# Optimization experiments

Hardware: AMD Instinct MI355X
Metric: run time of the kernel (lower is better)

## Reference

```python
import jax, jax.numpy as jnp
import numpy as np

N_NODES = 50000
N_EDGES = 800000
F_IN = 128
HID = 128
N_CLASSES = 16
N_GRAPHS = 64


def _glorot(key, shape):
    fan_in, fan_out = shape[0], shape[1]
    lim = (6.0 / (fan_in + fan_out)) ** 0.5
    return jax.random.uniform(key, shape, jnp.float32, -lim, lim)


def setup_inputs() -> dict:
    key = jax.random.key(0)
    ks = jax.random.split(key, 12)
    x = jax.random.normal(ks[0], (N_NODES, F_IN), jnp.float32)
    edge_index = jax.random.randint(ks[1], (2, N_EDGES), 0, N_NODES, jnp.int64)
    batch = jnp.sort(jax.random.randint(ks[2], (N_NODES,), 0, N_GRAPHS, jnp.int64))
    W0 = _glorot(ks[3], (F_IN, HID)); b0 = jnp.zeros((HID,), jnp.float32)
    W1 = _glorot(ks[4], (HID, HID)); b1 = jnp.zeros((HID,), jnp.float32)
    W2 = _glorot(ks[5], (HID, HID)); b2 = jnp.zeros((HID,), jnp.float32)
    Wc = _glorot(ks[6], (HID, N_CLASSES)); bc = jnp.zeros((N_CLASSES,), jnp.float32)
    return {"x": x, "edge_index": edge_index, "batch": batch,
            "W0": W0, "b0": b0, "W1": W1, "b1": b1, "W2": W2, "b2": b2,
            "Wc": Wc, "bc": bc}


def _gcn_prep(edge_index, n_nodes):
    # add self-loops, compute symmetric normalization coefficients
    loop = jnp.arange(n_nodes, dtype=edge_index.dtype)
    src = jnp.concatenate([edge_index[0], loop])
    dst = jnp.concatenate([edge_index[1], loop])
    deg = jax.ops.segment_sum(jnp.ones_like(dst, jnp.float32), dst, num_segments=n_nodes)
    dinv = deg ** -0.5  # deg >= 1 due to self-loops
    norm = dinv[src] * dinv[dst]  # [E+N]
    return src, dst, norm


def _gcn_layer(h, W, b, src, dst, norm, n_nodes):
    h = h @ W                                   # [N, out]
    msg = h[src] * norm[:, None]                # gather + scale [E+N, out]
    out = jax.ops.segment_sum(msg, dst, num_segments=n_nodes)  # scatter-add
    return out + b


def reference(x, edge_index, batch, W0, b0, W1, b1, W2, b2, Wc, bc):
    n = x.shape[0]
    src, dst, norm = _gcn_prep(edge_index, n)
    h = _gcn_layer(x, W0, b0, src, dst, norm, n)
    h = jax.nn.relu(h)  # dropout is identity in eval mode
    h = _gcn_layer(h, W1, b1, src, dst, norm, n)
    h = jax.nn.relu(h)
    h = _gcn_layer(h, W2, b2, src, dst, norm, n)
    # scatter-mean pooling over batch ids
    sums = jax.ops.segment_sum(h, batch, num_segments=N_GRAPHS)        # [G, HID]
    cnts = jax.ops.segment_sum(jnp.ones((n,), jnp.float32), batch, num_segments=N_GRAPHS)
    pooled = sums / jnp.maximum(cnts, 1.0)[:, None]
    return pooled @ Wc + bc  # [G, N_CLASSES]
```

## Files before the change

### kernel.cpp

```cpp
#include <hip/hip_runtime.h>
#include <hip/hip_bf16.h>
#include <hip/hip_fp16.h>

#define HID 128
#define NCLS 16
#define NGRAPH 64
#define CHUNK 1024

using bf16x8 = __attribute__((ext_vector_type(8))) short;
using f32x4  = __attribute__((ext_vector_type(4))) float;

__device__ __forceinline__ unsigned int f2bf(float f) {
    unsigned int u = __float_as_uint(f);
    return (u + 0x7FFFu + ((u >> 16) & 1u)) >> 16;
}
__device__ __forceinline__ float bf2f_lo(unsigned int u) { return __uint_as_float(u << 16); }
__device__ __forceinline__ float bf2f_hi(unsigned int u) { return __uint_as_float(u & 0xFFFF0000u); }

__global__ __launch_bounds__(256) void k_init(int* counts, float* pooled,
                                              const float* __restrict__ W0,
                                              const float* __restrict__ W1,
                                              const float* __restrict__ W2,
                                              const float* __restrict__ Wc,
                                              const float* __restrict__ b2,
                                              const float* __restrict__ bcin,
                                              unsigned short* __restrict__ Wt,
                                              unsigned short* __restrict__ Wt2c,
                                              float* __restrict__ bc2, int n) {
    int i = blockIdx.x * 256 + threadIdx.x;
    if (i < n) counts[i] = 0;
    if (i < NGRAPH * NCLS) pooled[i] = 0.0f;
    if (i < 2 * HID * HID) {
        int m = i >> 14;
        int r = i & 16383;
        int c = r >> 7, k = r & 127;
        const float* W = (m == 0) ? W0 : W1;
        Wt[i] = (unsigned short)f2bf(W[k * HID + c]);
    }
    if (i < HID * NCLS) {
        int k = i >> 4, c = i & 15;
        float s = 0.f;
        #pragma unroll 8
        for (int j = 0; j < HID; ++j)
            s = fmaf(W2[k * HID + j], Wc[j * NCLS + c], s);
        Wt2c[c * 128 + k] = (unsigned short)f2bf(s);
    }
    if (i < NCLS) {
        float s = 0.f;
        for (int j = 0; j < HID; ++j)
            s = fmaf(b2[j], Wc[j * NCLS + i], s);
        bc2[i] = s + bcin[i];
    }
}

__global__ __launch_bounds__(256) void k_hist(const int* __restrict__ dst,
                                              int* counts, int* rank, int e) {
    int i = blockIdx.x * 256 + threadIdx.x;
    if (i < e) rank[i] = atomicAdd(&counts[dst[i]], 1);
}

__global__ __launch_bounds__(256) void k_chunksum(const int* __restrict__ counts,
                                                  int* csum, int n) {
    __shared__ int sdata[256];
    int b = blockIdx.x, t = threadIdx.x;
    int base = b * CHUNK + t * 4;
    int s = 0;
    #pragma unroll
    for (int j = 0; j < 4; ++j) { int i = base + j; if (i < n) s += counts[i]; }
    sdata[t] = s; __syncthreads();
    for (int off = 128; off > 0; off >>= 1) {
        if (t < off) sdata[t] += sdata[t + off];
        __syncthreads();
    }
    if (t == 0) csum[b] = sdata[0];
}

__global__ __launch_bounds__(256) void k_rowptr(const int* __restrict__ counts,
                                                const int* __restrict__ csum,
                                                int* rowptr, int n, int e) {
    __shared__ int sincl[256];
    __shared__ int s_coff;
    int b = blockIdx.x, t = threadIdx.x;
    if (t < 64) {
        int v = (t < b) ? csum[t] : 0;
        #pragma unroll
        for (int off = 32; off > 0; off >>= 1) v += __shfl_xor(v, off);
        if (t == 0) s_coff = v;
    }
    int base = b * CHUNK + t * 4;
    int v[4]; int s = 0;
    #pragma unroll
    for (int j = 0; j < 4; ++j) { int i = base + j; v[j] = (i < n) ? counts[i] : 0; s += v[j]; }
    sincl[t] = s; __syncthreads();
    for (int off = 1; off < 256; off <<= 1) {
        int x = sincl[t];
        int y = (t >= off) ? sincl[t - off] : 0;
        __syncthreads();
        sincl[t] = x + y;
        __syncthreads();
    }
    int run = s_coff + sincl[t] - s;
    #pragma unroll
    for (int j = 0; j < 4; ++j) {
        int i = base + j;
        if (i < n) { rowptr[i] = run; run += v[j]; }
    }
    if (b == 0 && t == 0) rowptr[n] = e;
}

__global__ __launch_bounds__(256) void k_fill(const int* __restrict__ src,
                                              const int* __restrict__ dst,
                                              const int* __restrict__ rank,
                                              const int* __restrict__ counts,
                                              const int* __restrict__ rowptr,
                                              unsigned int* __restrict__ epk, int e) {
    int i = blockIdx.x * 256 + threadIdx.x;
    if (i >= e) return;
    int s = src[i], d = dst[i];
    int pos = rowptr[d] + rank[i];
    float norm = rsqrtf((float)(counts[s] + 1)) * rsqrtf((float)(counts[d] + 1));
    __half h = __float2half(norm);
    unsigned int hu = (unsigned int)__half_as_ushort(h);
    epk[pos] = (unsigned int)s | (hu << 16);
}

__global__ __launch_bounds__(256) void k_gemm_f32(const float* __restrict__ H,
                                                  const unsigned short* __restrict__ Wt,
                                                  unsigned short* __restrict__ Tb16, int n) {
    __shared__ char ldsA[64 * 256];
    int t = threadIdx.x;
    int cg = t & 31;
    int rg = t >> 5;
    int row0 = blockIdx.x * 64;

    #pragma unroll
    for (int i = 0; i < 8; ++i) {
        int lr = rg + i * 8;
        int r = row0 + lr;
        float4 v = make_float4(0.f, 0.f, 0.f, 0.f);
        if (r < n) v = ((const float4*)H)[(size_t)r * 32 + cg];
        uint2 pk;
        pk.x = f2bf(v.x) | (f2bf(v.y) << 16);
        pk.y = f2bf(v.z) | (f2bf(v.w) << 16);
        int byte = lr * 256 + cg * 8;
        *(uint2*)(ldsA + (byte ^ ((lr & 7) << 4))) = pk;
    }
    __syncthreads();

    int lane = t & 63;
    int w = t >> 6;
    int rsub = lane & 15;
    int kg = lane >> 4;
    int rowIdx = w * 16 + rsub;
    int abase = rowIdx * 256 + kg * 16;
    int aswz = (rowIdx & 7) << 4;

    f32x4 acc[8];
    #pragma unroll
    for (int nt = 0; nt < 8; ++nt) acc[nt] = (f32x4)(0.f);

    #pragma unroll
    for (int kk = 0; kk < 4; ++kk) {
        bf16x8 a = *(const bf16x8*)(ldsA + ((abase + kk * 64) ^ aswz));
        int k0 = kk * 32 + kg * 8;
        #pragma unroll
        for (int nt = 0; nt < 8; ++nt) {
            int col = nt * 16 + rsub;
            bf16x8 b = *(const bf16x8*)(Wt + col * 128 + k0);
            acc[nt] = __builtin_amdgcn_mfma_f32_16x16x32_bf16(a, b, acc[nt], 0, 0, 0);
        }
    }

    #pragma unroll
    for (int nt = 0; nt < 8; ++nt) {
        #pragma unroll
        for (int j = 0; j < 4; ++j) {
            int row = row0 + w * 16 + kg * 4 + j;
            int col = nt * 16 + rsub;
            if (row < n) Tb16[(size_t)row * 128 + col] = (unsigned short)f2bf(acc[nt][j]);
        }
    }
}

__global__ __launch_bounds__(256) void k_gemm_bf16(const unsigned short* __restrict__ Hb,
                                                   const unsigned short* __restrict__ Wt,
                                                   unsigned short* __restrict__ Tb16, int n) {
    __shared__ char ldsA[64 * 256];
    int t = threadIdx.x;
    int row0 = blockIdx.x * 64;
    int c16 = t & 15;
    int rbase = t >> 4;

    #pragma unroll
    for (int i = 0; i < 4; ++i) {
        int lr = rbase + i * 16;
        int r = row0 + lr;
        uint4 v = make_uint4(0u, 0u, 0u, 0u);
        if (r < n) v = *(const uint4*)(Hb + (size_t)r * 128 + c16 * 8);
        int byte = lr * 256 + c16 * 16;
        *(uint4*)(ldsA + (byte ^ ((lr & 7) << 4))) = v;
    }
    __syncthreads();

    int lane = t & 63;
    int w = t >> 6;
    int rsub = lane & 15;
    int kg = lane >> 4;
    int rowIdx = w * 16 + rsub;
    int abase = rowIdx * 256 + kg * 16;
    int aswz = (rowIdx & 7) << 4;

    f32x4 acc[8];
    #pragma unroll
    for (int nt = 0; nt < 8; ++nt) acc[nt] = (f32x4)(0.f);

    #pragma unroll
    for (int kk = 0; kk < 4; ++kk) {
        bf16x8 a = *(const bf16x8*)(ldsA + ((abase + kk * 64) ^ aswz));
        int k0 = kk * 32 + kg * 8;
        #pragma unroll
        for (int nt = 0; nt < 8; ++nt) {
            int col = nt * 16 + rsub;
            bf16x8 b = *(const bf16x8*)(Wt + col * 128 + k0);
            acc[nt] = __builtin_amdgcn_mfma_f32_16x16x32_bf16(a, b, acc[nt], 0, 0, 0);
        }
    }

    #pragma unroll
    for (int nt = 0; nt < 8; ++nt) {
        #pragma unroll
        for (int j = 0; j < 4; ++j) {
            int row = row0 + w * 16 + kg * 4 + j;
            int col = nt * 16 + rsub;
            if (row < n) Tb16[(size_t)row * 128 + col] = (unsigned short)f2bf(acc[nt][j]);
        }
    }
}

__global__ __launch_bounds__(256) void k_agg(const unsigned int* __restrict__ Tb,
                                             unsigned int* __restrict__ outB,
                                             const int* __restrict__ rowptr,
                                             const unsigned int* __restrict__ epk,
                                             const float* __restrict__ bias, int n) {
    int wid = (blockIdx.x * 256 + threadIdx.x) >> 6;
    int lane = threadIdx.x & 63;
    if (wid >= n) return;
    float2 b2 = ((const float2*)bias)[lane];
    unsigned int us = Tb[(size_t)wid * 64 + lane];
    int start = rowptr[wid];
    int deg = rowptr[wid + 1] - start;
    float sn = 1.0f / (float)(deg + 1);
    float2 acc;
    acc.x = fmaf(bf2f_lo(us), sn, b2.x);
    acc.y = fmaf(bf2f_hi(us), sn, b2.y);

    for (int j0 = 0; j0 < deg; j0 += 64) {
        int myj = j0 + lane;
        unsigned int rec = 0;
        if (myj < deg) rec = epk[start + myj];
        int m = min(64, deg - j0);
        int jj = 0;
        for (; jj + 16 <= m; jj += 16) {
            unsigned int rr[16], uu[16];
            #pragma unroll
            for (int k = 0; k < 16; ++k) rr[k] = (unsigned int)__shfl((int)rec, jj + k);
            #pragma unroll
            for (int k = 0; k < 16; ++k) uu[k] = Tb[(size_t)(rr[k] & 0xFFFFu) * 64 + lane];
            #pragma unroll
            for (int k = 0; k < 16; ++k) {
                float wk = __half2float(__ushort_as_half((unsigned short)(rr[k] >> 16)));
                acc.x = fmaf(wk, bf2f_lo(uu[k]), acc.x);
                acc.y = fmaf(wk, bf2f_hi(uu[k]), acc.y);
            }
        }
        for (; jj + 4 <= m; jj += 4) {
            unsigned int rr[4], uu[4];
            #pragma unroll
            for (int k = 0; k < 4; ++k) rr[k] = (unsigned int)__shfl((int)rec, jj + k);
            #pragma unroll
            for (int k = 0; k < 4; ++k) uu[k] = Tb[(size_t)(rr[k] & 0xFFFFu) * 64 + lane];
            #pragma unroll
            for (int k = 0; k < 4; ++k) {
                float wk = __half2float(__ushort_as_half((unsigned short)(rr[k] >> 16)));
                acc.x = fmaf(wk, bf2f_lo(uu[k]), acc.x);
                acc.y = fmaf(wk, bf2f_hi(uu[k]), acc.y);
            }
        }
        for (; jj < m; ++jj) {
            unsigned int rj = (unsigned int)__shfl((int)rec, jj);
            unsigned int u = Tb[(size_t)(rj & 0xFFFFu) * 64 + lane];
            float wj = __half2float(__ushort_as_half((unsigned short)(rj >> 16)));
            acc.x = fmaf(wj, bf2f_lo(u), acc.x);
            acc.y = fmaf(wj, bf2f_hi(u), acc.y);
        }
    }

    float rx = fmaxf(acc.x, 0.f), ry = fmaxf(acc.y, 0.f);
    outB[(size_t)wid * 64 + lane] = f2bf(rx) | (f2bf(ry) << 16);
}

__global__ __launch_bounds__(256) void k_agg_fused(const unsigned int* __restrict__ Tb,
                                                   float* __restrict__ T16,
                                                   const int* __restrict__ rowptr,
                                                   const unsigned int* __restrict__ epk,
                                                   const float* __restrict__ bias,
                                                   const unsigned short* __restrict__ Wt2c,
                                                   int n) {
    int t = threadIdx.x;
    int wid = (blockIdx.x * 256 + t) >> 6;
    int lane = t & 63;
    int c = lane & 15;
    int half = lane >> 4;
    if (wid >= n) return;

    float2 acc;
    float2 b2 = ((const float2*)bias)[lane];
    unsigned int us = Tb[(size_t)wid * 64 + lane];
    int start = rowptr[wid];
    int deg = rowptr[wid + 1] - start;
    float sn = 1.0f / (float)(deg + 1);
    acc.x = fmaf(bf2f_lo(us), sn, b2.x);
    acc.y = fmaf(bf2f_hi(us), sn, b2.y);

    for (int j0 = 0; j0 < deg; j0 += 64) {
        int myj = j0 + lane;
        unsigned int rec = 0;
        if (myj < deg) rec = epk[start + myj];
        int m = min(64, deg - j0);
        int jj = 0;
        for (; jj + 16 <= m; jj += 16) {
            unsigned int rr[16], uu[16];
            #pragma unroll
            for (int k = 0; k < 16; ++k) rr[k] = (unsigned int)__shfl((int)rec, jj + k);
            #pragma unroll
            for (int k = 0; k < 16; ++k) uu[k] = Tb[(size_t)(rr[k] & 0xFFFFu) * 64 + lane];
            #pragma unroll
            for (int k = 0; k < 16; ++k) {
                float wk = __half2float(__ushort_as_half((unsigned short)(rr[k] >> 16)));
                acc.x = fmaf(wk, bf2f_lo(uu[k]), acc.x);
                acc.y = fmaf(wk, bf2f_hi(uu[k]), acc.y);
            }
        }
        for (; jj + 4 <= m; jj += 4) {
            unsigned int rr[4], uu[4];
            #pragma unroll
            for (int k = 0; k < 4; ++k) rr[k] = (unsigned int)__shfl((int)rec, jj + k);
            #pragma unroll
            for (int k = 0; k < 4; ++k) uu[k] = Tb[(size_t)(rr[k] & 0xFFFFu) * 64 + lane];
            #pragma unroll
            for (int k = 0; k < 4; ++k) {
                float wk = __half2float(__ushort_as_half((unsigned short)(rr[k] >> 16)));
                acc.x = fmaf(wk, bf2f_lo(uu[k]), acc.x);
                acc.y = fmaf(wk, bf2f_hi(uu[k]), acc.y);
            }
        }
        for (; jj < m; ++jj) {
            unsigned int rj = (unsigned int)__shfl((int)rec, jj);
            unsigned int u = Tb[(size_t)(rj & 0xFFFFu) * 64 + lane];
            float wj = __half2float(__ushort_as_half((unsigned short)(rj >> 16)));
            acc.x = fmaf(wj, bf2f_lo(u), acc.x);
            acc.y = fmaf(wj, bf2f_hi(u), acc.y);
        }
    }

    float rx = fmaxf(acc.x, 0.f), ry = fmaxf(acc.y, 0.f);
    unsigned int hv = f2bf(rx) | (f2bf(ry) << 16);

    const uint4* wq = (const uint4*)((const unsigned int*)Wt2c + (c * 64 + half * 16));
    uint4 wv0 = wq[0], wv1 = wq[1], wv2 = wq[2], wv3 = wq[3];

    float part = 0.f;
    #pragma unroll
    for (int kk = 0; kk < 4; ++kk) {
        unsigned int hu = (unsigned int)__shfl((int)hv, half * 16 + kk);
        unsigned int wu = (&wv0.x)[kk];
        part = fmaf(bf2f_lo(hu), bf2f_lo(wu), part);
        part = fmaf(bf2f_hi(hu), bf2f_hi(wu), part);
    }
    #pragma unroll
    for (int kk = 0; kk < 4; ++kk) {
        unsigned int hu = (unsigned int)__shfl((int)hv, half * 16 + 4 + kk);
        unsigned int wu = (&wv1.x)[kk];
        part = fmaf(bf2f_lo(hu), bf2f_lo(wu), part);
        part = fmaf(bf2f_hi(hu), bf2f_hi(wu), part);
    }
    #pragma unroll
    for (int kk = 0; kk < 4; ++kk) {
        unsigned int hu = (unsigned int)__shfl((int)hv, half * 16 + 8 + kk);
        unsigned int wu = (&wv2.x)[kk];
        part = fmaf(bf2f_lo(hu), bf2f_lo(wu), part);
        part = fmaf(bf2f_hi(hu), bf2f_hi(wu), part);
    }
    #pragma unroll
    for (int kk = 0; kk < 4; ++kk) {
        unsigned int hu = (unsigned int)__shfl((int)hv, half * 16 + 12 + kk);
        unsigned int wu = (&wv3.x)[kk];
        part = fmaf(bf2f_lo(hu), bf2f_lo(wu), part);
        part = fmaf(bf2f_hi(hu), bf2f_hi(wu), part);
    }
    part += __shfl_xor(part, 16);
    part += __shfl_xor(part, 32);

    if (half == 0) T16[(size_t)wid * 16 + c] = part;
}

__global__ __launch_bounds__(256) void k_agg16(const float* __restrict__ T16,
                                               float* __restrict__ G16,
                                               const int* __restrict__ rowptr,
                                               const unsigned int* __restrict__ epk, int n) {
    int wid = (blockIdx.x * 256 + threadIdx.x) >> 6;
    int lane = threadIdx.x & 63;
    if (wid >= n) return;
    int p = lane & 15;
    int q = lane >> 4;
    int start = rowptr[wid];
    int deg = rowptr[wid + 1] - start;

    float acc = 0.f;
    if (q == 0) {
        float sn = 1.0f / (float)(deg + 1);
        acc = T16[(size_t)wid * 16 + p] * sn;
    }

    for (int j0 = 0; j0 < deg; j0 += 64) {
        int myj = j0 + lane;
        unsigned int rec = 0;
        if (myj < deg) rec = epk[start + myj];
        int m = min(64, deg - j0);
        int mg = (m - q + 3) >> 2;
        int jj = 0;
        for (; jj + 8 <= mg; jj += 8) {
            unsigned int rr[8]; float uu[8];
            #pragma unroll
            for (int k = 0; k < 8; ++k) rr[k] = (unsigned int)__shfl((int)rec, 4 * (jj + k) + q);
            #pragma unroll
            for (int k = 0; k < 8; ++k) uu[k] = T16[(size_t)(rr[k] & 0xFFFFu) * 16 + p];
            #pragma unroll
            for (int k = 0; k < 8; ++k) {
                float wk = __half2float(__ushort_as_half((unsigned short)(rr[k] >> 16)));
                acc = fmaf(wk, uu[k], acc);
            }
        }
        for (; jj < mg; ++jj) {
            unsigned int rj = (unsigned int)__shfl((int)rec, 4 * jj + q);
            float u = T16[(size_t)(rj & 0xFFFFu) * 16 + p];
            float wj = __half2float(__ushort_as_half((unsigned short)(rj >> 16)));
            acc = fmaf(wj, u, acc);
        }
    }

    acc += __shfl_xor(acc, 16);
    acc += __shfl_xor(acc, 32);

    if (q == 0) G16[(size_t)wid * 16 + p] = acc;
}

__global__ __launch_bounds__(256) void k_pool16(const float* __restrict__ G16,
                                                const int* __restrict__ batch,
                                                float* pooled, int n) {
    int gw = (blockIdx.x * 256 + threadIdx.x) >> 6;
    int lane = threadIdx.x & 63;
    int p = lane & 15;
    int q = lane >> 4;
    int n0 = gw * 64;
    if (n0 >= n) return;
    int n1 = min(n0 + 64, n);
    int i0 = n0 + q;
    if (i0 >= n1) return;
    int gprev = batch[i0];
    float acc = 0.f;
    for (int i = i0; i < n1; i += 4) {
        int g = batch[i];
        if (g != gprev) {
            atomicAdd(&pooled[gprev * NCLS + p], acc);
            acc = 0.f; gprev = g;
        }
        acc += G16[(size_t)i * 16 + p];
    }
    atomicAdd(&pooled[gprev * NCLS + p], acc);
}

__global__ __launch_bounds__(256) void k_head16(const float* __restrict__ pooled,
                                                const int* __restrict__ batch,
                                                const float* __restrict__ bc2,
                                                float* __restrict__ out, int n) {
    int idx = blockIdx.x * 256 + threadIdx.x;
    if (idx >= NGRAPH * NCLS) return;
    int g = idx >> 4, c = idx & 15;
    int lo = 0, hi = n;
    while (lo < hi) { int mid = (lo + hi) >> 1; if (batch[mid] < g) lo = mid + 1; else hi = mid; }
    int lb = lo;
    lo = 0; hi = n;
    while (lo < hi) { int mid = (lo + hi) >> 1; if (batch[mid] < g + 1) lo = mid + 1; else hi = mid; }
    float cnt = (float)(lo - lb);
    float inv = 1.0f / fmaxf(cnt, 1.0f);
    out[idx] = pooled[idx] * inv + bc2[c];
}

extern "C" void kernel_launch(void* const* d_in, const int* in_sizes, int n_in,
                              void* d_out, int out_size, void* d_ws, size_t ws_size,
                              hipStream_t stream) {
    const float* x    = (const float*)d_in[0];
    const int*   ei   = (const int*)d_in[1];
    const int*   batch= (const int*)d_in[2];
    const float* W0   = (const float*)d_in[3];
    const float* b0   = (const float*)d_in[4];
    const float* W1   = (const float*)d_in[5];
    const float* b1   = (const float*)d_in[6];
    const float* W2   = (const float*)d_in[7];
    const float* b2   = (const float*)d_in[8];
    const float* Wc   = (const float*)d_in[9];
    const float* bc   = (const float*)d_in[10];
    float* out = (float*)d_out;

    const int N = in_sizes[0] / HID;
    const int E = in_sizes[1] / 2;
    const int* src = ei;
    const int* dst = ei + E;

    char* p = (char*)d_ws;
    auto alloc = [&](size_t bytes) { void* r = (void*)p; p += (bytes + 255) & ~(size_t)255; return r; };
    int*   counts = (int*)alloc((size_t)N * 4);
    int*   rank   = (int*)alloc((size_t)E * 4);
    int*   csum   = (int*)alloc(256 * 4);
    int*   rowptr = (int*)alloc((size_t)(N + 1) * 4);
    unsigned int* epk = (unsigned int*)alloc((size_t)E * 4);
    float* pooled = (float*)alloc((size_t)NGRAPH * NCLS * 4);
    unsigned short* Tb16 = (unsigned short*)alloc((size_t)N * HID * 2);
    unsigned short* Hb16 = (unsigned short*)alloc((size_t)N * HID * 2);
    float* T16    = (float*)alloc((size_t)N * NCLS * 4);
    float* G16    = (float*)alloc((size_t)N * NCLS * 4);
    unsigned short* Wt   = (unsigned short*)alloc((size_t)2 * HID * HID * 2);
    unsigned short* Wt2c = (unsigned short*)alloc((size_t)NCLS * 128 * 2);
    float* bc2    = (float*)alloc(NCLS * 4);

    const int NB = (N + CHUNK - 1) / CHUNK;

    k_init<<<(N + 255) / 256, 256, 0, stream>>>(counts, pooled, W0, W1, W2, Wc, b2, bc,
                                                Wt, Wt2c, bc2, N);
    k_hist<<<(E + 255) / 256, 256, 0, stream>>>(dst, counts, rank, E);
    k_chunksum<<<NB, 256, 0, stream>>>(counts, csum, N);
    k_rowptr<<<NB, 256, 0, stream>>>(counts, csum, rowptr, N, E);
    k_fill<<<(E + 255) / 256, 256, 0, stream>>>(src, dst, rank, counts, rowptr, epk, E);

    const int gemm_grid = (N + 63) / 64;
    const int agg_grid  = ((size_t)N * 64 + 255) / 256;

    k_gemm_f32<<<gemm_grid, 256, 0, stream>>>(x, Wt, Tb16, N);
    k_agg<<<agg_grid, 256, 0, stream>>>((const unsigned int*)Tb16, (unsigned int*)Hb16,
                                        rowptr, epk, b0, N);
    k_gemm_bf16<<<gemm_grid, 256, 0, stream>>>(Hb16, Wt + 16384, Tb16, N);
    k_agg_fused<<<agg_grid, 256, 0, stream>>>((const unsigned int*)Tb16, T16,
                                              rowptr, epk, b1, Wt2c, N);
    k_agg16<<<agg_grid, 256, 0, stream>>>(T16, G16, rowptr, epk, N);
    const int pool_blocks = (((N + 63) / 64) * 64 + 255) / 256;
    k_pool16<<<pool_blocks, 256, 0, stream>>>(G16, batch, pooled, N);
    k_head16<<<(NGRAPH * NCLS + 255) / 256, 256, 0, stream>>>(pooled, batch, bc2, out, N);
}
```

Measured before the change: 230.1 us.

## Split 128-wide aggregation rows across four lane groups with 16-byte gathers

Rewrites the two 128-channel aggregation kernels so each wavefront splits into four 16-lane groups. Each group gathers a different neighbor's full 256-byte bf16 row with uint4 loads, and the partial sums are combined with xor shuffles. This aims to put four independent neighbor gathers in flight per instruction and to widen the memory accesses compared with one neighbor per step using 4-byte loads. The cost is more registers, cross-lane reductions, and padding records when the degree is not a multiple of four, which rely on zero weights. The fused 16-class projection is reorganized to match the new layout.

```diff
diff --git a/kernel.cpp b/kernel.cpp
--- a/kernel.cpp
+++ b/kernel.cpp
@@ -16,6 +16,9 @@
 }
 __device__ __forceinline__ float bf2f_lo(unsigned int u) { return __uint_as_float(u << 16); }
 __device__ __forceinline__ float bf2f_hi(unsigned int u) { return __uint_as_float(u & 0xFFFF0000u); }
+__device__ __forceinline__ float h2f(unsigned int rec) {
+    return __half2float(__ushort_as_half((unsigned short)(rec >> 16)));
+}
 
 __global__ __launch_bounds__(256) void k_init(int* counts, float* pooled,
                                               const float* __restrict__ W0,
@@ -237,171 +240,201 @@
     }
 }
 
-__global__ __launch_bounds__(256) void k_agg(const unsigned int* __restrict__ Tb,
-                                             unsigned int* __restrict__ outB,
+__global__ __launch_bounds__(256) void k_agg(const uint4* __restrict__ Tb4,
+                                             uint4* __restrict__ outB4,
                                              const int* __restrict__ rowptr,
                                              const unsigned int* __restrict__ epk,
-                                             const float* __restrict__ bias, int n) {
+                                             const float4* __restrict__ bias4, int n) {
     int wid = (blockIdx.x * 256 + threadIdx.x) >> 6;
     int lane = threadIdx.x & 63;
     if (wid >= n) return;
-    float2 b2 = ((const float2*)bias)[lane];
-    unsigned int us = Tb[(size_t)wid * 64 + lane];
+    int p = lane & 15;
+    int q = lane >> 4;
     int start = rowptr[wid];
     int deg = rowptr[wid + 1] - start;
-    float sn = 1.0f / (float)(deg + 1);
-    float2 acc;
-    acc.x = fmaf(bf2f_lo(us), sn, b2.x);
-    acc.y = fmaf(bf2f_hi(us), sn, b2.y);
+
+    float2 acc[4];
+    #pragma unroll
+    for (int i = 0; i < 4; ++i) acc[i] = make_float2(0.f, 0.f);
+    if (q == 0) {
+        float sn = 1.0f / (float)(deg + 1);
+        uint4 us = Tb4[(size_t)wid * 16 + p];
+        float4 bA = bias4[p * 2], bB = bias4[p * 2 + 1];
+        acc[0].x = fmaf(bf2f_lo(us.x), sn, bA.x);
+        acc[0].y = fmaf(bf2f_hi(us.x), sn, bA.y);
+        acc[1].x = fmaf(bf2f_lo(us.y), sn, bA.z);
+        acc[1].y = fmaf(bf2f_hi(us.y), sn, bA.w);
+        acc[2].x = fmaf(bf2f_lo(us.z), sn, bB.x);
+        acc[2].y = fmaf(bf2f_hi(us.z), sn, bB.y);
+        acc[3].x = fmaf(bf2f_lo(us.w), sn, bB.z);
+        acc[3].y = fmaf(bf2f_hi(us.w), sn, bB.w);
+    }
 
     for (int j0 = 0; j0 < deg; j0 += 64) {
         int myj = j0 + lane;
         unsigned int rec = 0;
         if (myj < deg) rec = epk[start + myj];
         int m = min(64, deg - j0);
+        int mg = (m + 3) >> 2;
         int jj = 0;
-        for (; jj + 16 <= m; jj += 16) {
-            unsigned int rr[16], uu[16];
-            #pragma unroll
-            for (int k = 0; k < 16; ++k) rr[k] = (unsigned int)__shfl((int)rec, jj + k);
-            #pragma unroll
-            for (int k = 0; k < 16; ++k) uu[k] = Tb[(size_t)(rr[k] & 0xFFFFu) * 64 + lane];
-            #pragma unroll
-            for (int k = 0; k < 16; ++k) {
-                float wk = __half2float(__ushort_as_half((unsigned short)(rr[k] >> 16)));
-                acc.x = fmaf(wk, bf2f_lo(uu[k]), acc.x);
-                acc.y = fmaf(wk, bf2f_hi(uu[k]), acc.y);
+        for (; jj + 4 <= mg; jj += 4) {
+            unsigned int rr[4]; uint4 uu[4];
+            #pragma unroll
+            for (int k = 0; k < 4; ++k) rr[k] = (unsigned int)__shfl((int)rec, 4 * (jj + k) + q);
+            #pragma unroll
+            for (int k = 0; k < 4; ++k) uu[k] = Tb4[(size_t)(rr[k] & 0xFFFFu) * 16 + p];
+            #pragma unroll
+            for (int k = 0; k < 4; ++k) {
+                float wk = h2f(rr[k]);
+                acc[0].x = fmaf(wk, bf2f_lo(uu[k].x), acc[0].x);
+                acc[0].y = fmaf(wk, bf2f_hi(uu[k].x), acc[0].y);
+                acc[1].x = fmaf(wk, bf2f_lo(uu[k].y), acc[1].x);
+                acc[1].y = fmaf(wk, bf2f_hi(uu[k].y), acc[1].y);
+                acc[2].x = fmaf(wk, bf2f_lo(uu[k].z), acc[2].x);
+                acc[2].y = fmaf(wk, bf2f_hi(uu[k].z), acc[2].y);
+                acc[3].x = fmaf(wk, bf2f_lo(uu[k].w), acc[3].x);
+                acc[3].y = fmaf(wk, bf2f_hi(uu[k].w), acc[3].y);
             }
         }
-        for (; jj + 4 <= m; jj += 4) {
-            unsigned int rr[4], uu[4];
-            #pragma unroll
-            for (int k = 0; k < 4; ++k) rr[k] = (unsigned int)__shfl((int)rec, jj + k);
-            #pragma unroll
-            for (int k = 0; k < 4; ++k) uu[k] = Tb[(size_t)(rr[k] & 0xFFFFu) * 64 + lane];
-            #pragma unroll
-            for (int k = 0; k < 4; ++k) {
-                float wk = __half2float(__ushort_as_half((unsigned short)(rr[k] >> 16)));
-                acc.x = fmaf(wk, bf2f_lo(uu[k]), acc.x);
-                acc.y = fmaf(wk, bf2f_hi(uu[k]), acc.y);
-            }
-        }
-        for (; jj < m; ++jj) {
-            unsigned int rj = (unsigned int)__shfl((int)rec, jj);
-            unsigned int u = Tb[(size_t)(rj & 0xFFFFu) * 64 + lane];
-            float wj = __half2float(__ushort_as_half((unsigned short)(rj >> 16)));
-            acc.x = fmaf(wj, bf2f_lo(u), acc.x);
-            acc.y = fmaf(wj, bf2f_hi(u), acc.y);
-        }
-    }
-
-    float rx = fmaxf(acc.x, 0.f), ry = fmaxf(acc.y, 0.f);
-    outB[(size_t)wid * 64 + lane] = f2bf(rx) | (f2bf(ry) << 16);
-}
-
-__global__ __launch_bounds__(256) void k_agg_fused(const unsigned int* __restrict__ Tb,
+        for (; jj < mg; ++jj) {
+            unsigned int rj = (unsigned int)__shfl((int)rec, 4 * jj + q);
+            uint4 u = Tb4[(size_t)(rj & 0xFFFFu) * 16 + p];
+            float wj = h2f(rj);
+            acc[0].x = fmaf(wj, bf2f_lo(u.x), acc[0].x);
+            acc[0].y = fmaf(wj, bf2f_hi(u.x), acc[0].y);
+            acc[1].x = fmaf(wj, bf2f_lo(u.y), acc[1].x);
+            acc[1].y = fmaf(wj, bf2f_hi(u.y), acc[1].y);
+            acc[2].x = fmaf(wj, bf2f_lo(u.z), acc[2].x);
+            acc[2].y = fmaf(wj, bf2f_hi(u.z), acc[2].y);
+            acc[3].x = fmaf(wj, bf2f_lo(u.w), acc[3].x);
+            acc[3].y = fmaf(wj, bf2f_hi(u.w), acc[3].y);
+        }
+    }
+
+    #pragma unroll
+    for (int i = 0; i < 4; ++i) {
+        acc[i].x += __shfl_xor(acc[i].x, 16); acc[i].y += __shfl_xor(acc[i].y, 16);
+        acc[i].x += __shfl_xor(acc[i].x, 32); acc[i].y += __shfl_xor(acc[i].y, 32);
+    }
+
+    if (q == 0) {
+        uint4 o;
+        o.x = f2bf(fmaxf(acc[0].x, 0.f)) | (f2bf(fmaxf(acc[0].y, 0.f)) << 16);
+        o.y = f2bf(fmaxf(acc[1].x, 0.f)) | (f2bf(fmaxf(acc[1].y, 0.f)) << 16);
+        o.z = f2bf(fmaxf(acc[2].x, 0.f)) | (f2bf(fmaxf(acc[2].y, 0.f)) << 16);
+        o.w = f2bf(fmaxf(acc[3].x, 0.f)) | (f2bf(fmaxf(acc[3].y, 0.f)) << 16);
+        outB4[(size_t)wid * 16 + p] = o;
+    }
+}
+
+__global__ __launch_bounds__(256) void k_agg_fused(const uint4* __restrict__ Tb4,
                                                    float* __restrict__ T16,
                                                    const int* __restrict__ rowptr,
                                                    const unsigned int* __restrict__ epk,
-                                                   const float* __restrict__ bias,
+                                                   const float4* __restrict__ bias4,
                                                    const unsigned short* __restrict__ Wt2c,
                                                    int n) {
-    int t = threadIdx.x;
-    int wid = (blockIdx.x * 256 + t) >> 6;
-    int lane = t & 63;
-    int c = lane & 15;
-    int half = lane >> 4;
+    int wid = (blockIdx.x * 256 + threadIdx.x) >> 6;
+    int lane = threadIdx.x & 63;
     if (wid >= n) return;
-
-    float2 acc;
-    float2 b2 = ((const float2*)bias)[lane];
-    unsigned int us = Tb[(size_t)wid * 64 + lane];
+    int p = lane & 15;
+    int q = lane >> 4;
     int start = rowptr[wid];
     int deg = rowptr[wid + 1] - start;
-    float sn = 1.0f / (float)(deg + 1);
-    acc.x = fmaf(bf2f_lo(us), sn, b2.x);
-    acc.y = fmaf(bf2f_hi(us), sn, b2.y);
+
+    float2 acc[4];
+    #pragma unroll
+    for (int i = 0; i < 4; ++i) acc[i] = make_float2(0.f, 0.f);
+    if (q == 0) {
+        float sn = 1.0f / (float)(deg + 1);
+        uint4 us = Tb4[(size_t)wid * 16 + p];
+        float4 bA = bias4[p * 2], bB = bias4[p * 2 + 1];
+        acc[0].x = fmaf(bf2f_lo(us.x), sn, bA.x);
+        acc[0].y = fmaf(bf2f_hi(us.x), sn, bA.y);
+        acc[1].x = fmaf(bf2f_lo(us.y), sn, bA.z);
+        acc[1].y = fmaf(bf2f_hi(us.y), sn, bA.w);
+        acc[2].x = fmaf(bf2f_lo(us.z), sn, bB.x);
+        acc[2].y = fmaf(bf2f_hi(us.z), sn, bB.y);
+        acc[3].x = fmaf(bf2f_lo(us.w), sn, bB.z);
+        acc[3].y = fmaf(bf2f_hi(us.w), sn, bB.w);
+    }
 
     for (int j0 = 0; j0 < deg; j0 += 64) {
         int myj = j0 + lane;
         unsigned int rec = 0;
         if (myj < deg) rec = epk[start + myj];
         int m = min(64, deg - j0);
+        int mg = (m + 3) >> 2;
         int jj = 0;
-        for (; jj + 16 <= m; jj += 16) {
-            unsigned int rr[16], uu[16];
-            #pragma unroll
-            for (int k = 0; k < 16; ++k) rr[k] = (unsigned int)__shfl((int)rec, jj + k);
-            #pragma unroll
-            for (int k = 0; k < 16; ++k) uu[k] = Tb[(size_t)(rr[k] & 0xFFFFu) * 64 + lane];
-            #pragma unroll
-            for (int k = 0; k < 16; ++k) {
-                float wk = __half2float(__ushort_as_half((unsigned short)(rr[k] >> 16)));
-                acc.x = fmaf(wk, bf2f_lo(uu[k]), acc.x);
-                acc.y = fmaf(wk, bf2f_hi(uu[k]), acc.y);
+        for (; jj + 4 <= mg; jj += 4) {
+            unsigned int rr[4]; uint4 uu[4];
+            #pragma unroll
+            for (int k = 0; k < 4; ++k) rr[k] = (unsigned int)__shfl((int)rec, 4 * (jj + k) + q);
+            #pragma unroll
+            for (int k = 0; k < 4; ++k) uu[k] = Tb4[(size_t)(rr[k] & 0xFFFFu) * 16 + p];
+            #pragma unroll
+            for (int k = 0; k < 4; ++k) {
+                float wk = h2f(rr[k]);
+                acc[0].x = fmaf(wk, bf2f_lo(uu[k].x), acc[0].x);
+                acc[0].y = fmaf(wk, bf2f_hi(uu[k].x), acc[0].y);
+                acc[1].x = fmaf(wk, bf2f_lo(uu[k].y), acc[1].x);
+                acc[1].y = fmaf(wk, bf2f_hi(uu[k].y), acc[1].y);
+                acc[2].x = fmaf(wk, bf2f_lo(uu[k].z), acc[2].x);
+                acc[2].y = fmaf(wk, bf2f_hi(uu[k].z), acc[2].y);
+                acc[3].x = fmaf(wk, bf2f_lo(uu[k].w), acc[3].x);
+                acc[3].y = fmaf(wk, bf2f_hi(uu[k].w), acc[3].y);
             }
         }
-        for (; jj + 4 <= m; jj += 4) {
-            unsigned int rr[4], uu[4];
-            #pragma unroll
-            for (int k = 0; k < 4; ++k) rr[k] = (unsigned int)__shfl((int)rec, jj + k);
-            #pragma unroll
-            for (int k = 0; k < 4; ++k) uu[k] = Tb[(size_t)(rr[k] & 0xFFFFu) * 64 + lane];
-            #pragma unroll
-            for (int k = 0; k < 4; ++k) {
-                float wk = __half2float(__ushort_as_half((unsigned short)(rr[k] >> 16)));
-                acc.x = fmaf(wk, bf2f_lo(uu[k]), acc.x);
-                acc.y = fmaf(wk, bf2f_hi(uu[k]), acc.y);
-            }
-        }
-        for (; jj < m; ++jj) {
-            unsigned int rj = (unsigned int)__shfl((int)rec, jj);
-            unsigned int u = Tb[(size_t)(rj & 0xFFFFu) * 64 + lane];
-            float wj = __half2float(__ushort_as_half((unsigned short)(rj >> 16)));
-            acc.x = fmaf(wj, bf2f_lo(u), acc.x);
-            acc.y = fmaf(wj, bf2f_hi(u), acc.y);
-        }
-    }
-
-    float rx = fmaxf(acc.x, 0.f), ry = fmaxf(acc.y, 0.f);
-    unsigned int hv = f2bf(rx) | (f2bf(ry) << 16);
-
-    const uint4* wq = (const uint4*)((const unsigned int*)Wt2c + (c * 64 + half * 16));
-    uint4 wv0 = wq[0], wv1 = wq[1], wv2 = wq[2], wv3 = wq[3];
-
+        for (; jj < mg; ++jj) {
+            unsigned int rj = (unsigned int)__shfl((int)rec, 4 * jj + q);
+            uint4 u = Tb4[(size_t)(rj & 0xFFFFu) * 16 + p];
+            float wj = h2f(rj);
+            acc[0].x = fmaf(wj, bf2f_lo(u.x), acc[0].x);
+            acc[0].y = fmaf(wj, bf2f_hi(u.x), acc[0].y);
+            acc[1].x = fmaf(wj, bf2f_lo(u.y), acc[1].x);
+            acc[1].y = fmaf(wj, bf2f_hi(u.y), acc[1].y);
+            acc[2].x = fmaf(wj, bf2f_lo(u.z), acc[2].x);
+            acc[2].y = fmaf(wj, bf2f_hi(u.z), acc[2].y);
+            acc[3].x = fmaf(wj, bf2f_lo(u.w), acc[3].x);
+            acc[3].y = fmaf(wj, bf2f_hi(u.w), acc[3].y);
+        }
+    }
+
+    #pragma unroll
+    for (int i = 0; i < 4; ++i) {
+        acc[i].x += __shfl_xor(acc[i].x, 16); acc[i].y += __shfl_xor(acc[i].y, 16);
+        acc[i].x += __shfl_xor(acc[i].x, 32); acc[i].y += __shfl_xor(acc[i].y, 32);
+    }
+
+    uint4 hv;
+    hv.x = f2bf(fmaxf(acc[0].x, 0.f)) | (f2bf(fmaxf(acc[0].y, 0.f)) << 16);
+    hv.y = f2bf(fmaxf(acc[1].x, 0.f)) | (f2bf(fmaxf(acc[1].y, 0.f)) << 16);
+    hv.z = f2bf(fmaxf(acc[2].x, 0.f)) | (f2bf(fmaxf(acc[2].y, 0.f)) << 16);
+    hv.w = f2bf(fmaxf(acc[3].x, 0.f)) | (f2bf(fmaxf(acc[3].y, 0.f)) << 16);
+
+    int c = p;
     float part = 0.f;
     #pragma unroll
-    for (int kk = 0; kk < 4; ++kk) {
-        unsigned int hu = (unsigned int)__shfl((int)hv, half * 16 + kk);
-        unsigned int wu = (&wv0.x)[kk];
-        part = fmaf(bf2f_lo(hu), bf2f_lo(wu), part);
-        part = fmaf(bf2f_hi(hu), bf2f_hi(wu), part);
-    }
-    #pragma unroll
-    for (int kk = 0; kk < 4; ++kk) {
-        unsigned int hu = (unsigned int)__shfl((int)hv, half * 16 + 4 + kk);
-        unsigned int wu = (&wv1.x)[kk];
-        part = fmaf(bf2f_lo(hu), bf2f_lo(wu), part);
-        part = fmaf(bf2f_hi(hu), bf2f_hi(wu), part);
-    }
-    #pragma unroll
-    for (int kk = 0; kk < 4; ++kk) {
-        unsigned int hu = (unsigned int)__shfl((int)hv, half * 16 + 8 + kk);
-        unsigned int wu = (&wv2.x)[kk];
-        part = fmaf(bf2f_lo(hu), bf2f_lo(wu), part);
-        part = fmaf(bf2f_hi(hu), bf2f_hi(wu), part);
-    }
-    #pragma unroll
-    for (int kk = 0; kk < 4; ++kk) {
-        unsigned int hu = (unsigned int)__shfl((int)hv, half * 16 + 12 + kk);
-        unsigned int wu = (&wv3.x)[kk];
-        part = fmaf(bf2f_lo(hu), bf2f_lo(wu), part);
-        part = fmaf(bf2f_hi(hu), bf2f_hi(wu), part);
+    for (int s = 0; s < 4; ++s) {
+        int ps = q + s * 4;
+        unsigned int h0 = (unsigned int)__shfl((int)hv.x, ps);
+        unsigned int h1 = (unsigned int)__shfl((int)hv.y, ps);
+        unsigned int h2 = (unsigned int)__shfl((int)hv.z, ps);
+        unsigned int h3 = (unsigned int)__shfl((int)hv.w, ps);
+        uint4 wv = ((const uint4*)Wt2c)[c * 16 + ps];
+        part = fmaf(bf2f_lo(h0), bf2f_lo(wv.x), part);
+        part = fmaf(bf2f_hi(h0), bf2f_hi(wv.x), part);
+        part = fmaf(bf2f_lo(h1), bf2f_lo(wv.y), part);
+        part = fmaf(bf2f_hi(h1), bf2f_hi(wv.y), part);
+        part = fmaf(bf2f_lo(h2), bf2f_lo(wv.z), part);
+        part = fmaf(bf2f_hi(h2), bf2f_hi(wv.z), part);
+        part = fmaf(bf2f_lo(h3), bf2f_lo(wv.w), part);
+        part = fmaf(bf2f_hi(h3), bf2f_hi(wv.w), part);
     }
     part += __shfl_xor(part, 16);
     part += __shfl_xor(part, 32);
 
-    if (half == 0) T16[(size_t)wid * 16 + c] = part;
+    if (q == 0) T16[(size_t)wid * 16 + c] = part;
 }
 
 __global__ __launch_bounds__(256) void k_agg16(const float* __restrict__ T16,
@@ -427,7 +460,7 @@
         unsigned int rec = 0;
         if (myj < deg) rec = epk[start + myj];
         int m = min(64, deg - j0);
-        int mg = (m - q + 3) >> 2;
+        int mg = (m + 3) >> 2;
         int jj = 0;
         for (; jj + 8 <= mg; jj += 8) {
             unsigned int rr[8]; float uu[8];
@@ -436,16 +469,12 @@
             #pragma unroll
             for (int k = 0; k < 8; ++k) uu[k] = T16[(size_t)(rr[k] & 0xFFFFu) * 16 + p];
             #pragma unroll
-            for (int k = 0; k < 8; ++k) {
-                float wk = __half2float(__ushort_as_half((unsigned short)(rr[k] >> 16)));
-                acc = fmaf(wk, uu[k], acc);
-            }
+            for (int k = 0; k < 8; ++k) acc = fmaf(h2f(rr[k]), uu[k], acc);
         }
         for (; jj < mg; ++jj) {
             unsigned int rj = (unsigned int)__shfl((int)rec, 4 * jj + q);
             float u = T16[(size_t)(rj & 0xFFFFu) * 16 + p];
-            float wj = __half2float(__ushort_as_half((unsigned short)(rj >> 16)));
-            acc = fmaf(wj, u, acc);
+            acc = fmaf(h2f(rj), u, acc);
         }
     }
 
@@ -547,11 +576,11 @@
     const int agg_grid  = ((size_t)N * 64 + 255) / 256;
 
     k_gemm_f32<<<gemm_grid, 256, 0, stream>>>(x, Wt, Tb16, N);
-    k_agg<<<agg_grid, 256, 0, stream>>>((const unsigned int*)Tb16, (unsigned int*)Hb16,
-                                        rowptr, epk, b0, N);
+    k_agg<<<agg_grid, 256, 0, stream>>>((const uint4*)Tb16, (uint4*)Hb16,
+                                        rowptr, epk, (const float4*)b0, N);
     k_gemm_bf16<<<gemm_grid, 256, 0, stream>>>(Hb16, Wt + 16384, Tb16, N);
-    k_agg_fused<<<agg_grid, 256, 0, stream>>>((const unsigned int*)Tb16, T16,
-                                              rowptr, epk, b1, Wt2c, N);
+    k_agg_fused<<<agg_grid, 256, 0, stream>>>((const uint4*)Tb16, T16,
+                                              rowptr, epk, (const float4*)b1, Wt2c, N);
     k_agg16<<<agg_grid, 256, 0, stream>>>(T16, G16, rowptr, epk, N);
     const int pool_blocks = (((N + 63) / 64) * 64 + 255) / 256;
     k_pool16<<<pool_blocks, 256, 0, stream>>>(G16, batch, pooled, N);
```

After: 228.2 us. Within noise of the previous version (-0.8%).
